# Kernel tuning notes

Measured on AMD Instinct MI355X. Metric: run time of the kernel, lower is better.

## Reference

```python
import jax, jax.numpy as jnp
import numpy as np

NUM_NODES = 10000
IN_DIM = 128
GAT_UNITS = 64
K = 20  # min(20, num_nodes - 1)
NEG_SLOPE = 0.2


def setup_inputs() -> dict:
    key = jax.random.key(0)
    ks = jax.random.split(key, 10)
    s = lambda k, shape, scale: jax.random.normal(k, shape, jnp.float32) * scale
    return {
        "x": s(ks[0], (NUM_NODES, IN_DIM), 1.0),
        "emb": s(ks[1], (NUM_NODES, 16), 1.0),
        "W1": s(ks[2], (IN_DIM, 4, GAT_UNITS), 0.05),
        "a1_src": s(ks[3], (4, GAT_UNITS), 0.05),
        "a1_tgt": s(ks[4], (4, GAT_UNITS), 0.05),
        "b1": jnp.zeros((4 * GAT_UNITS,), jnp.float32),
        "W2": s(ks[5], (4 * GAT_UNITS, 1, GAT_UNITS), 0.05),
        "a2_src": s(ks[6], (1, GAT_UNITS), 0.05),
        "a2_tgt": s(ks[7], (1, GAT_UNITS), 0.05),
        "b2": jnp.zeros((GAT_UNITS,), jnp.float32),
    }


def _build_edges(emb):
    # top-k adjacency from cosine similarity of node embeddings
    norm = emb / jnp.linalg.norm(emb, axis=-1, keepdims=True)
    sim = norm @ norm.T                      # [N, N]
    _, idx = jax.lax.top_k(sim, K)           # [N, K]
    n = emb.shape[0]
    src = jnp.repeat(jnp.arange(n, dtype=jnp.int32), K)
    tgt = idx.reshape(-1).astype(jnp.int32)
    # append self loops (as in the original module)
    loop = jnp.arange(n, dtype=jnp.int32)
    src = jnp.concatenate([src, loop])
    tgt = jnp.concatenate([tgt, loop])
    return src, tgt                          # each [N*(K+1)]


def _gat(x, W, a_src, a_tgt, src, tgt, n):
    # x: [N, F]; W: [F, H, C]; a_*: [H, C]
    h = jnp.einsum("nf,fhc->nhc", x, W)      # [N, H, C]
    e_src = jnp.einsum("nhc,hc->nh", h, a_src)  # [N, H]
    e_tgt = jnp.einsum("nhc,hc->nh", h, a_tgt)  # [N, H]
    logits = jax.nn.leaky_relu(e_src[src] + e_tgt[tgt], NEG_SLOPE)  # [E, H]
    # segment softmax over each source node's neighborhood
    m = jax.ops.segment_max(logits, src, num_segments=n)
    ex = jnp.exp(logits - m[src])
    z = jax.ops.segment_sum(ex, src, num_segments=n)
    alpha = ex / z[src]                      # [E, H]
    msg = alpha[:, :, None] * h[tgt]         # [E, H, C]
    return jax.ops.segment_sum(msg, src, num_segments=n)  # [N, H, C]


def reference(x, emb, W1, a1_src, a1_tgt, b1, W2, a2_src, a2_tgt, b2):
    n = x.shape[0]
    src, tgt = _build_edges(emb)
    # GAT layer 1: 4 heads, concatenated
    h1 = _gat(x, W1, a1_src, a1_tgt, src, tgt, n)        # [N, 4, C]
    h1 = h1.reshape(n, -1) + b1                           # [N, 4C]
    h1 = jax.nn.relu(h1)                                  # (dropout: inference mode)
    # GAT layer 2: 1 head, no concat
    h2 = _gat(h1, W2, a2_src, a2_tgt, src, tgt, n)        # [N, 1, C]
    return h2[:, 0, :] + b2                               # [N, C]
```

## Files before the change

### kernel.cpp

```cpp
#include <hip/hip_runtime.h>
#include <math.h>


#define N_NODES 10000
#define EMB_D   16
#define IN_DIM  128
#define H1      4
#define CDIM    64
#define D1      256
#define K_TOP   20
#define NEIGH   21
#define SROWS   32
#define NTILES  313
#define NTP     320
#define JSPLIT  2
#define HALFT   160
#define CAPM    128
#define GUARD   0.016f

typedef __attribute__((ext_vector_type(8)))  short short8;
typedef __attribute__((ext_vector_type(16))) float f32x16;

__device__ __forceinline__ unsigned monokey(float v) {
  unsigned u = __float_as_uint(v);
  return (u & 0x80000000u) ? ~u : (u | 0x80000000u);
}
__device__ __forceinline__ float invmono(unsigned m) {
  unsigned u = (m & 0x80000000u) ? (m ^ 0x80000000u) : ~m;
  return __uint_as_float(u);
}
__device__ __forceinline__ unsigned short f32_to_bf16(float f) {
  unsigned u = __float_as_uint(f);
  unsigned r = 0x7FFFu + ((u >> 16) & 1u);
  return (unsigned short)((u + r) >> 16);
}

__device__ __forceinline__ float dot16q(float4 qa, float4 qb, float4 qc, float4 qd,
                                        float4 v0, float4 v1, float4 v2, float4 v3) {
  float a = 0.f;
  a = fmaf(qa.x, v0.x, a); a = fmaf(qa.y, v0.y, a);
  a = fmaf(qa.z, v0.z, a); a = fmaf(qa.w, v0.w, a);
  a = fmaf(qb.x, v1.x, a); a = fmaf(qb.y, v1.y, a);
  a = fmaf(qb.z, v1.z, a); a = fmaf(qb.w, v1.w, a);
  a = fmaf(qc.x, v2.x, a); a = fmaf(qc.y, v2.y, a);
  a = fmaf(qc.z, v2.z, a); a = fmaf(qc.w, v2.w, a);
  a = fmaf(qd.x, v3.x, a); a = fmaf(qd.y, v3.y, a);
  a = fmaf(qd.z, v3.z, a); a = fmaf(qd.w, v3.w, a);
  return a;
}

__global__ __launch_bounds__(256) void normalize_kernel(
    const float* __restrict__ emb, float* __restrict__ nrm,
    unsigned short* __restrict__ nrmh) {
  int i = blockIdx.x * 256 + threadIdx.x;
  if (i >= N_NODES) return;
  const float4* p = (const float4*)(emb + (size_t)i * EMB_D);
  float4 v[4];
  float ss = 0.f;
#pragma unroll
  for (int k = 0; k < 4; k++) {
    v[k] = p[k];
    ss = fmaf(v[k].x, v[k].x, ss);
    ss = fmaf(v[k].y, v[k].y, ss);
    ss = fmaf(v[k].z, v[k].z, ss);
    ss = fmaf(v[k].w, v[k].w, ss);
  }
  float nv = sqrtf(ss);
  float4* o = (float4*)(nrm + (size_t)i * EMB_D);
  ushort4* oh = (ushort4*)(nrmh + (size_t)i * EMB_D);
#pragma unroll
  for (int k = 0; k < 4; k++) {
    float4 t;
    t.x = v[k].x / nv; t.y = v[k].y / nv; t.z = v[k].z / nv; t.w = v[k].w / nv;
    o[k] = t;
    ushort4 h;
    h.x = f32_to_bf16(t.x); h.y = f32_to_bf16(t.y);
    h.z = f32_to_bf16(t.z); h.w = f32_to_bf16(t.w);
    oh[k] = h;
  }
}

__global__ __launch_bounds__(512) void sim_topk_part(
    const float* __restrict__ nrm, const unsigned short* __restrict__ nrmh,
    unsigned long long* __restrict__ pkeys) {
  __shared__ unsigned short s_qbf[SROWS * EMB_D];
  __shared__ float s_qf[SROWS * EMB_D];
  __shared__ __align__(16) char s_ovl[SROWS * 256 * 4];
  float (*s_smax)[256] = (float(*)[256])s_ovl;
  unsigned long long (*s_ckey)[CAPM] = (unsigned long long(*)[CAPM])s_ovl;
  __shared__ int s_cid[SROWS][CAPM];
  __shared__ float s_thr[SROWS];
  __shared__ int s_cnt[SROWS];

  int tid = threadIdx.x;
  int w = tid >> 6, lane = tid & 63;
  int lo5 = lane & 31, hi = lane >> 5;
  int row0 = blockIdx.x * SROWS;
  int bh = blockIdx.y;
  int tbase = bh * HALFT;

  if (tid < SROWS * EMB_D) {
    int gi = row0 * EMB_D + tid;
    float v = (gi < N_NODES * EMB_D) ? nrm[gi] : 0.f;
    s_qf[tid] = v;
    s_qbf[tid] = f32_to_bf16(v);
  }
  if (tid < SROWS) s_cnt[tid] = 0;
  __syncthreads();

  short8 afrag = *(const short8*)&s_qbf[lo5 * EMB_D + hi * 8];
  const f32x16 zacc = (f32x16)0.0f;

  float rm[16];
#pragma unroll
  for (int r = 0; r < 16; r++) rm[r] = -INFINITY;

#pragma unroll
  for (int g = 0; g < 5; ++g) {
    int tb = tbase + g * 32 + w * 4;
    int nd[4];
    short8 bf[4];
#pragma unroll
    for (int u = 0; u < 4; u++) {
      nd[u] = (tb + u) * 32 + lo5;
      bf[u] = (short8)(short)0;
      if (nd[u] < N_NODES)
        bf[u] = *(const short8*)&nrmh[(size_t)nd[u] * EMB_D + hi * 8];
    }
#pragma unroll
    for (int u = 0; u < 4; u++) {
      f32x16 acc = __builtin_amdgcn_mfma_f32_32x32x16_bf16(afrag, bf[u], zacc, 0, 0, 0);
      if (nd[u] < N_NODES) {
#pragma unroll
        for (int r = 0; r < 16; r++) rm[r] = fmaxf(rm[r], acc[r]);
      }
    }
  }
#pragma unroll
  for (int r = 0; r < 16; r++) {
    int rl = (r & 3) + 8 * (r >> 2) + 4 * hi;
    s_smax[rl][w * 32 + lo5] = rm[r];
  }
  __syncthreads();

  for (int q = 0; q < 4; q++) {
    int row = w * 4 + q;
    float m01 = fmaxf(s_smax[row][lane], s_smax[row][64 + lane]);
    float m23 = fmaxf(s_smax[row][128 + lane], s_smax[row][192 + lane]);
    unsigned v = monokey(fmaxf(m01, m23));
#pragma unroll
    for (int k = 2; k <= 64; k <<= 1) {
#pragma unroll
      for (int j = k >> 1; j > 0; j >>= 1) {
        unsigned o = __shfl_xor(v, j);
        bool upper = (lane & j) != 0;
        bool ascend = (lane & k) == 0;
        unsigned mx = v > o ? v : o;
        unsigned mn = v > o ? o : v;
        v = (upper == ascend) ? mx : mn;
      }
    }
    unsigned t20 = __shfl(v, 44);
    if (lane == 0)
      s_thr[row] = (row0 + row < N_NODES) ? invmono(t20) - GUARD : INFINITY;
  }
  __syncthreads();

  float thr_r[16];
#pragma unroll
  for (int r = 0; r < 16; r++)
    thr_r[r] = s_thr[(r & 3) + 8 * (r >> 2) + 4 * hi];

#pragma unroll
  for (int g = 0; g < 5; ++g) {
    int tb = tbase + g * 32 + w * 4;
    int nd[4];
    short8 bf[4];
#pragma unroll
    for (int u = 0; u < 4; u++) {
      nd[u] = (tb + u) * 32 + lo5;
      bf[u] = (short8)(short)0;
      if (nd[u] < N_NODES)
        bf[u] = *(const short8*)&nrmh[(size_t)nd[u] * EMB_D + hi * 8];
    }
#pragma unroll
    for (int u = 0; u < 4; u++) {
      f32x16 acc = __builtin_amdgcn_mfma_f32_32x32x16_bf16(afrag, bf[u], zacc, 0, 0, 0);
      if (nd[u] < N_NODES) {
#pragma unroll
        for (int r = 0; r < 16; r++) {
          if (acc[r] >= thr_r[r]) {
            int rl = (r & 3) + 8 * (r >> 2) + 4 * hi;
            int slot = atomicAdd(&s_cnt[rl], 1);
            if (slot < CAPM) s_cid[rl][slot] = nd[u];
          }
        }
      }
    }
  }
  __syncthreads();

  for (int q = 0; q < 4; q++) {
    int row = w * 4 + q;
    if (row0 + row >= N_NODES) continue;
    int M = s_cnt[row];
    if (M > CAPM) continue;
    const float4* qp = (const float4*)&s_qf[row * EMB_D];
    float4 qa = qp[0], qb = qp[1], qc = qp[2], qd = qp[3];
    for (int c = lane; c < M; c += 64) {
      int id = s_cid[row][c];
      const float4* pj = (const float4*)(nrm + (size_t)id * EMB_D);
      float sim = dot16q(qa, qb, qc, qd, pj[0], pj[1], pj[2], pj[3]);
      s_ckey[row][c] = ((unsigned long long)monokey(sim) << 32) |
                       (unsigned long long)(0xFFFFFFFFu - (unsigned)id);
    }
  }
  __syncthreads();

  for (int q = 0; q < 4; q++) {
    int row = w * 4 + q;
    int grow = row0 + row;
    if (grow >= N_NODES) continue;
    unsigned long long* outp = pkeys + ((size_t)grow * JSPLIT + bh) * K_TOP;
    int M = s_cnt[row];
    if (M <= CAPM) {
      for (int c = lane; c < M; c += 64) {
        unsigned long long mykey = s_ckey[row][c];
        int rank = 0;
        for (int i = 0; i < M; i++) rank += (s_ckey[row][i] > mykey) ? 1 : 0;
        if (rank < K_TOP) outp[rank] = mykey;
      }
    } else {
      const float4* qp = (const float4*)&s_qf[row * EMB_D];
      float4 qa = qp[0], qb = qp[1], qc = qp[2], qd = qp[3];
      int j0 = tbase * 32;
      int jend = j0 + HALFT * 32; if (jend > N_NODES) jend = N_NODES;
      unsigned long long prev = ~0ull;
      for (int r = 0; r < K_TOP; r++) {
        unsigned long long best = 0ull;
        for (int j = j0 + lane; j < jend; j += 64) {
          const float4* pj = (const float4*)(nrm + (size_t)j * EMB_D);
          float sim = dot16q(qa, qb, qc, qd, pj[0], pj[1], pj[2], pj[3]);
          unsigned long long key = ((unsigned long long)monokey(sim) << 32) |
                                   (unsigned long long)(0xFFFFFFFFu - (unsigned)j);
          if (key < prev && key > best) best = key;
        }
#pragma unroll
        for (int off = 32; off > 0; off >>= 1) {
          unsigned long long o = __shfl_down(best, off);
          if (o > best) best = o;
        }
        best = __shfl(best, 0);
        prev = best;
        if (lane == 0) outp[r] = best;
      }
    }
  }
}

__global__ __launch_bounds__(256) void topk_merge(
    const unsigned long long* __restrict__ pkeys, int* __restrict__ topk) {
  __shared__ unsigned long long s_k[4][JSPLIT * K_TOP];
  int w = threadIdx.x >> 6, lane = threadIdx.x & 63;
  int row = blockIdx.x * 4 + w;
  const unsigned long long* src = pkeys + (size_t)row * (JSPLIT * K_TOP);
  if (lane < JSPLIT * K_TOP) s_k[w][lane] = src[lane];
  __syncthreads();
  if (lane < JSPLIT * K_TOP) {
    unsigned long long mykey = s_k[w][lane];
    int rank = 0;
    for (int i = 0; i < JSPLIT * K_TOP; i++)
      rank += (s_k[w][i] > mykey) ? 1 : 0;
    if (rank < K_TOP)
      topk[(size_t)row * K_TOP + rank] =
          (int)(0xFFFFFFFFu - (unsigned)(mykey & 0xFFFFFFFFull));
  }
}

__global__ __launch_bounds__(512) void gemm1_kernel(
    const float* __restrict__ A, const float* __restrict__ B,
    const float* __restrict__ a_src, const float* __restrict__ a_tgt,
    float* __restrict__ Cc, float* __restrict__ es, float* __restrict__ et) {
  __shared__ float As[16][IN_DIM];
  int r0 = blockIdx.x * 16;
  int tid = threadIdx.y * 256 + threadIdx.x;
  {
    int rr = tid >> 5;
    int kk = tid & 31;
    ((float4*)&As[rr][0])[kk] = ((const float4*)(A + (size_t)(r0 + rr) * IN_DIM))[kk];
  }
  __syncthreads();
  int col = threadIdx.x;
  int y = threadIdx.y;
  float acc[8] = {0, 0, 0, 0, 0, 0, 0, 0};
#pragma unroll 4
  for (int k = 0; k < IN_DIM; k++) {
    float bv = B[(size_t)k * D1 + col];
#pragma unroll
    for (int r = 0; r < 8; r++) acc[r] = fmaf(As[y * 8 + r][k], bv, acc[r]);
  }
#pragma unroll
  for (int r = 0; r < 8; r++)
    Cc[(size_t)(r0 + y * 8 + r) * D1 + col] = acc[r];
  float as = a_src[col], at = a_tgt[col];
  int h = col >> 6;
#pragma unroll
  for (int r = 0; r < 8; r++) {
    float ps = acc[r] * as, pt = acc[r] * at;
#pragma unroll
    for (int off = 32; off > 0; off >>= 1) {
      ps += __shfl_down(ps, off);
      pt += __shfl_down(pt, off);
    }
    if ((col & 63) == 0) {
      es[(size_t)(r0 + y * 8 + r) * H1 + h] = ps;
      et[(size_t)(r0 + y * 8 + r) * H1 + h] = pt;
    }
  }
}

__global__ __launch_bounds__(256) void gemm2_kernel(
    const float* __restrict__ A, const float* __restrict__ B,
    const float* __restrict__ a_src, const float* __restrict__ a_tgt,
    float* __restrict__ Cc, float* __restrict__ es, float* __restrict__ et) {
  __shared__ float As[16][D1];
  int r0 = blockIdx.x * 16;
  int tid = threadIdx.y * 64 + threadIdx.x;
  for (int e = tid; e < 16 * (D1 / 4); e += 256) {
    int rr = e >> 6;
    int kk = e & 63;
    ((float4*)&As[rr][0])[kk] = ((const float4*)(A + (size_t)(r0 + rr) * D1))[kk];
  }
  __syncthreads();
  int col = threadIdx.x;
  int y = threadIdx.y;
  float acc[4] = {0, 0, 0, 0};
#pragma unroll 4
  for (int k = 0; k < D1; k++) {
    float bv = B[(size_t)k * CDIM + col];
#pragma unroll
    for (int r = 0; r < 4; r++) acc[r] = fmaf(As[y * 4 + r][k], bv, acc[r]);
  }
#pragma unroll
  for (int r = 0; r < 4; r++)
    Cc[(size_t)(r0 + y * 4 + r) * CDIM + col] = acc[r];
  float as = a_src[col], at = a_tgt[col];
#pragma unroll
  for (int r = 0; r < 4; r++) {
    float ps = acc[r] * as, pt = acc[r] * at;
#pragma unroll
    for (int off = 32; off > 0; off >>= 1) {
      ps += __shfl_down(ps, off);
      pt += __shfl_down(pt, off);
    }
    if (col == 0) {
      es[r0 + y * 4 + r] = ps;
      et[r0 + y * 4 + r] = pt;
    }
  }
}

__global__ __launch_bounds__(256) void agg1_kernel(
    const float* __restrict__ h1p, const float* __restrict__ es,
    const float* __restrict__ et, const int* __restrict__ topk,
    const float* __restrict__ b1, float* __restrict__ h1o) {
  int i = blockIdx.x;
  int tid = threadIdx.x;
  __shared__ int nb[NEIGH];
  __shared__ float lg[NEIGH][H1];
  if (tid < K_TOP) nb[tid] = topk[(size_t)i * K_TOP + tid];
  else if (tid == K_TOP) nb[K_TOP] = i;
  __syncthreads();
  if (tid < NEIGH * H1) {
    int e = tid & 3, jj = tid >> 2;
    float L = es[(size_t)i * H1 + e] + et[(size_t)nb[jj] * H1 + e];
    lg[jj][e] = (L > 0.f) ? L : 0.2f * L;
  }
  __syncthreads();
  int h = tid >> 6;
  float m = -INFINITY;
#pragma unroll
  for (int jj = 0; jj < NEIGH; jj++) m = fmaxf(m, lg[jj][h]);
  float z = 0.f, acc = 0.f;
#pragma unroll
  for (int jj = 0; jj < NEIGH; jj++) {
    float w = expf(lg[jj][h] - m);
    z += w;
    acc = fmaf(w, h1p[(size_t)nb[jj] * D1 + tid], acc);
  }
  float o = acc / z + b1[tid];
  h1o[(size_t)i * D1 + tid] = fmaxf(o, 0.f);
}

__global__ __launch_bounds__(256) void agg2_kernel(
    const float* __restrict__ h2p, const float* __restrict__ es,
    const float* __restrict__ et, const int* __restrict__ topk,
    const float* __restrict__ b2, float* __restrict__ out) {
  int tid = threadIdx.x;
  int li = tid >> 6;
  int c = tid & 63;
  int i = blockIdx.x * 4 + li;
  __shared__ int nb[4][NEIGH];
  __shared__ float lg[4][NEIGH];
  if (tid < 4 * NEIGH) {
    int li2 = tid / NEIGH, jj = tid % NEIGH;
    int node = blockIdx.x * 4 + li2;
    nb[li2][jj] = (jj < K_TOP) ? topk[(size_t)node * K_TOP + jj] : node;
  }
  __syncthreads();
  if (tid < 4 * NEIGH) {
    int li2 = tid / NEIGH, jj = tid % NEIGH;
    int node = blockIdx.x * 4 + li2;
    float L = es[node] + et[nb[li2][jj]];
    lg[li2][jj] = (L > 0.f) ? L : 0.2f * L;
  }
  __syncthreads();
  float m = -INFINITY;
#pragma unroll
  for (int jj = 0; jj < NEIGH; jj++) m = fmaxf(m, lg[li][jj]);
  float z = 0.f, acc = 0.f;
#pragma unroll
  for (int jj = 0; jj < NEIGH; jj++) {
    float w = expf(lg[li][jj] - m);
    z += w;
    acc = fmaf(w, h2p[(size_t)nb[li][jj] * CDIM + c], acc);
  }
  out[(size_t)i * CDIM + c] = acc / z + b2[c];
}

extern "C" void kernel_launch(void* const* d_in, const int* in_sizes, int n_in,
                              void* d_out, int out_size, void* d_ws, size_t ws_size,
                              hipStream_t stream) {
  const float* x   = (const float*)d_in[0];
  const float* emb = (const float*)d_in[1];
  const float* W1  = (const float*)d_in[2];
  const float* a1s = (const float*)d_in[3];
  const float* a1t = (const float*)d_in[4];
  const float* b1  = (const float*)d_in[5];
  const float* W2  = (const float*)d_in[6];
  const float* a2s = (const float*)d_in[7];
  const float* a2t = (const float*)d_in[8];
  const float* b2  = (const float*)d_in[9];
  float* out = (float*)d_out;

  size_t off = 0;
  auto alloc = [&](size_t bytes) {
    void* p = (char*)d_ws + off;
    off += (bytes + 255) & ~(size_t)255;
    return p;
  };
  float*          nrm  = (float*)alloc((size_t)N_NODES * EMB_D * sizeof(float));
  unsigned short* nrmh = (unsigned short*)alloc((size_t)N_NODES * EMB_D * sizeof(unsigned short));
  int*   topk = (int*)  alloc((size_t)N_NODES * K_TOP * sizeof(int));
  float* h1p  = (float*)alloc((size_t)N_NODES * D1 * sizeof(float));
  float* e1s  = (float*)alloc((size_t)N_NODES * H1 * sizeof(float));
  float* e1t  = (float*)alloc((size_t)N_NODES * H1 * sizeof(float));
  float* h1   = (float*)alloc((size_t)N_NODES * D1 * sizeof(float));
  float* h2p  = (float*)alloc((size_t)N_NODES * CDIM * sizeof(float));
  float* e2s  = (float*)alloc((size_t)N_NODES * sizeof(float));
  float* e2t  = (float*)alloc((size_t)N_NODES * sizeof(float));
  unsigned long long* pkeys = (unsigned long long*)h1p;
  (void)ws_size; (void)in_sizes; (void)n_in; (void)out_size;

  normalize_kernel<<<(N_NODES + 255) / 256, 256, 0, stream>>>(emb, nrm, nrmh);
  sim_topk_part<<<dim3(NTILES, JSPLIT), 512, 0, stream>>>(nrm, nrmh, pkeys);
  topk_merge<<<N_NODES / 4, 256, 0, stream>>>(pkeys, topk);
  gemm1_kernel<<<N_NODES / 16, dim3(256, 2), 0, stream>>>(x, W1, a1s, a1t, h1p, e1s, e1t);
  agg1_kernel<<<N_NODES, 256, 0, stream>>>(h1p, e1s, e1t, topk, b1, h1);
  gemm2_kernel<<<N_NODES / 16, dim3(64, 4), 0, stream>>>(h1, W2, a2s, a2t, h2p, e2s, e2t);
  agg2_kernel<<<N_NODES / 4, 256, 0, stream>>>(h2p, e2s, e2t, topk, b2, out);
}
```

Baseline: 158.1 us.

## Fuse layer-1 aggregation into layer-2 GEMM and shrink top-k candidate LDS

```diff
diff --git a/kernel.cpp b/kernel.cpp
--- a/kernel.cpp
+++ b/kernel.cpp
@@ -12,10 +12,9 @@
 #define NEIGH   21
 #define SROWS   32
 #define NTILES  313
-#define NTP     320
 #define JSPLIT  2
 #define HALFT   160
-#define CAPM    128
+#define CAPM    96
 #define GUARD   0.016f
 
 typedef __attribute__((ext_vector_type(8)))  short short8;
@@ -85,10 +84,11 @@
     unsigned long long* __restrict__ pkeys) {
   __shared__ unsigned short s_qbf[SROWS * EMB_D];
   __shared__ float s_qf[SROWS * EMB_D];
-  __shared__ __align__(16) char s_ovl[SROWS * 256 * 4];
+  __shared__ __align__(16) char s_ovl[32768];
   float (*s_smax)[256] = (float(*)[256])s_ovl;
   unsigned long long (*s_ckey)[CAPM] = (unsigned long long(*)[CAPM])s_ovl;
-  __shared__ int s_cid[SROWS][CAPM];
+  unsigned short (*s_cid)[CAPM] =
+      (unsigned short(*)[CAPM])(s_ovl + 24576);
   __shared__ float s_thr[SROWS];
   __shared__ int s_cnt[SROWS];
 
@@ -192,7 +192,7 @@
           if (acc[r] >= thr_r[r]) {
             int rl = (r & 3) + 8 * (r >> 2) + 4 * hi;
             int slot = atomicAdd(&s_cnt[rl], 1);
-            if (slot < CAPM) s_cid[rl][slot] = nd[u];
+            if (slot < CAPM) s_cid[rl][slot] = (unsigned short)nd[u];
           }
         }
       }
@@ -293,11 +293,20 @@
   int col = threadIdx.x;
   int y = threadIdx.y;
   float acc[8] = {0, 0, 0, 0, 0, 0, 0, 0};
-#pragma unroll 4
-  for (int k = 0; k < IN_DIM; k++) {
-    float bv = B[(size_t)k * D1 + col];
-#pragma unroll
-    for (int r = 0; r < 8; r++) acc[r] = fmaf(As[y * 8 + r][k], bv, acc[r]);
+  for (int k4 = 0; k4 < IN_DIM / 4; k4++) {
+    float4 a[8];
+#pragma unroll
+    for (int r = 0; r < 8; r++) a[r] = ((const float4*)&As[y * 8 + r][0])[k4];
+    float bv[4];
+#pragma unroll
+    for (int i = 0; i < 4; i++) bv[i] = B[(size_t)(k4 * 4 + i) * D1 + col];
+#pragma unroll
+    for (int r = 0; r < 8; r++) {
+      acc[r] = fmaf(a[r].x, bv[0], acc[r]);
+      acc[r] = fmaf(a[r].y, bv[1], acc[r]);
+      acc[r] = fmaf(a[r].z, bv[2], acc[r]);
+      acc[r] = fmaf(a[r].w, bv[3], acc[r]);
+    }
   }
 #pragma unroll
   for (int r = 0; r < 8; r++)
@@ -319,35 +328,82 @@
   }
 }
 
-__global__ __launch_bounds__(256) void gemm2_kernel(
-    const float* __restrict__ A, const float* __restrict__ B,
+__global__ __launch_bounds__(256) void agg1_gemm2_kernel(
+    const float* __restrict__ h1p, const float* __restrict__ e1s,
+    const float* __restrict__ e1t, const int* __restrict__ topk,
+    const float* __restrict__ b1, const float* __restrict__ B2,
     const float* __restrict__ a_src, const float* __restrict__ a_tgt,
-    float* __restrict__ Cc, float* __restrict__ es, float* __restrict__ et) {
+    float* __restrict__ h2p, float* __restrict__ es, float* __restrict__ et) {
   __shared__ float As[16][D1];
+  __shared__ int nb[16][NEIGH];
+  __shared__ float wv[16][NEIGH][H1];
+  __shared__ float zz[16][H1];
   int r0 = blockIdx.x * 16;
-  int tid = threadIdx.y * 64 + threadIdx.x;
-  for (int e = tid; e < 16 * (D1 / 4); e += 256) {
-    int rr = e >> 6;
-    int kk = e & 63;
-    ((float4*)&As[rr][0])[kk] = ((const float4*)(A + (size_t)(r0 + rr) * D1))[kk];
-  }
-  __syncthreads();
-  int col = threadIdx.x;
-  int y = threadIdx.y;
-  float acc[4] = {0, 0, 0, 0};
-#pragma unroll 4
-  for (int k = 0; k < D1; k++) {
-    float bv = B[(size_t)k * CDIM + col];
-#pragma unroll
-    for (int r = 0; r < 4; r++) acc[r] = fmaf(As[y * 4 + r][k], bv, acc[r]);
+  int tid = threadIdx.x;
+
+  for (int idx = tid; idx < 16 * NEIGH; idx += 256) {
+    int n = idx / NEIGH, jj = idx % NEIGH;
+    nb[n][jj] = (jj < K_TOP) ? topk[(size_t)(r0 + n) * K_TOP + jj] : (r0 + n);
+  }
+  __syncthreads();
+  for (int idx = tid; idx < 16 * NEIGH * H1; idx += 256) {
+    int e = idx & 3, jj = (idx >> 2) % NEIGH, n = idx / (NEIGH * H1);
+    float L = e1s[(size_t)(r0 + n) * H1 + e] + e1t[(size_t)nb[n][jj] * H1 + e];
+    wv[n][jj][e] = (L > 0.f) ? L : 0.2f * L;
+  }
+  __syncthreads();
+  if (tid < 16 * H1) {
+    int n = tid >> 2, h = tid & 3;
+    float m = -INFINITY;
+#pragma unroll
+    for (int jj = 0; jj < NEIGH; jj++) m = fmaxf(m, wv[n][jj][h]);
+    float z = 0.f;
+#pragma unroll
+    for (int jj = 0; jj < NEIGH; jj++) {
+      float wt = expf(wv[n][jj][h] - m);
+      z += wt;
+      wv[n][jj][h] = wt;
+    }
+    zz[n][h] = z;
+  }
+  __syncthreads();
+  {
+    int h = tid >> 6;
+    float bv = b1[tid];
+    for (int n = 0; n < 16; n++) {
+      float acc = 0.f;
+#pragma unroll
+      for (int jj = 0; jj < NEIGH; jj++)
+        acc = fmaf(wv[n][jj][h], h1p[(size_t)nb[n][jj] * D1 + tid], acc);
+      float o = acc / zz[n][h] + bv;
+      As[n][tid] = fmaxf(o, 0.f);
+    }
+  }
+  __syncthreads();
+  int col = tid & 63, y = tid >> 6;
+  float acc4[4] = {0, 0, 0, 0};
+  for (int k4 = 0; k4 < D1 / 4; k4++) {
+    float4 a[4];
+#pragma unroll
+    for (int r = 0; r < 4; r++) a[r] = ((const float4*)&As[y * 4 + r][0])[k4];
+    float bv[4];
+#pragma unroll
+    for (int i = 0; i < 4; i++) bv[i] = B2[(size_t)(k4 * 4 + i) * CDIM + col];
+#pragma unroll
+    for (int r = 0; r < 4; r++) {
+      acc4[r] = fmaf(a[r].x, bv[0], acc4[r]);
+      acc4[r] = fmaf(a[r].y, bv[1], acc4[r]);
+      acc4[r] = fmaf(a[r].z, bv[2], acc4[r]);
+      acc4[r] = fmaf(a[r].w, bv[3], acc4[r]);
+    }
   }
 #pragma unroll
   for (int r = 0; r < 4; r++)
-    Cc[(size_t)(r0 + y * 4 + r) * CDIM + col] = acc[r];
+    h2p[(size_t)(r0 + y * 4 + r) * CDIM + col] = acc4[r];
   float as = a_src[col], at = a_tgt[col];
 #pragma unroll
   for (int r = 0; r < 4; r++) {
-    float ps = acc[r] * as, pt = acc[r] * at;
+    float ps = acc4[r] * as, pt = acc4[r] * at;
 #pragma unroll
     for (int off = 32; off > 0; off >>= 1) {
       ps += __shfl_down(ps, off);
@@ -358,38 +414,6 @@
       et[r0 + y * 4 + r] = pt;
     }
   }
-}
-
-__global__ __launch_bounds__(256) void agg1_kernel(
-    const float* __restrict__ h1p, const float* __restrict__ es,
-    const float* __restrict__ et, const int* __restrict__ topk,
-    const float* __restrict__ b1, float* __restrict__ h1o) {
-  int i = blockIdx.x;
-  int tid = threadIdx.x;
-  __shared__ int nb[NEIGH];
-  __shared__ float lg[NEIGH][H1];
-  if (tid < K_TOP) nb[tid] = topk[(size_t)i * K_TOP + tid];
-  else if (tid == K_TOP) nb[K_TOP] = i;
-  __syncthreads();
-  if (tid < NEIGH * H1) {
-    int e = tid & 3, jj = tid >> 2;
-    float L = es[(size_t)i * H1 + e] + et[(size_t)nb[jj] * H1 + e];
-    lg[jj][e] = (L > 0.f) ? L : 0.2f * L;
-  }
-  __syncthreads();
-  int h = tid >> 6;
-  float m = -INFINITY;
-#pragma unroll
-  for (int jj = 0; jj < NEIGH; jj++) m = fmaxf(m, lg[jj][h]);
-  float z = 0.f, acc = 0.f;
-#pragma unroll
-  for (int jj = 0; jj < NEIGH; jj++) {
-    float w = expf(lg[jj][h] - m);
-    z += w;
-    acc = fmaf(w, h1p[(size_t)nb[jj] * D1 + tid], acc);
-  }
-  float o = acc / z + b1[tid];
-  h1o[(size_t)i * D1 + tid] = fmaxf(o, 0.f);
 }
 
 __global__ __launch_bounds__(256) void agg2_kernel(
@@ -455,7 +479,6 @@
   float* h1p  = (float*)alloc((size_t)N_NODES * D1 * sizeof(float));
   float* e1s  = (float*)alloc((size_t)N_NODES * H1 * sizeof(float));
   float* e1t  = (float*)alloc((size_t)N_NODES * H1 * sizeof(float));
-  float* h1   = (float*)alloc((size_t)N_NODES * D1 * sizeof(float));
   float* h2p  = (float*)alloc((size_t)N_NODES * CDIM * sizeof(float));
   float* e2s  = (float*)alloc((size_t)N_NODES * sizeof(float));
   float* e2t  = (float*)alloc((size_t)N_NODES * sizeof(float));
@@ -466,7 +489,7 @@
   sim_topk_part<<<dim3(NTILES, JSPLIT), 512, 0, stream>>>(nrm, nrmh, pkeys);
   topk_merge<<<N_NODES / 4, 256, 0, stream>>>(pkeys, topk);
   gemm1_kernel<<<N_NODES / 16, dim3(256, 2), 0, stream>>>(x, W1, a1s, a1t, h1p, e1s, e1t);
-  agg1_kernel<<<N_NODES, 256, 0, stream>>>(h1p, e1s, e1t, topk, b1, h1);
-  gemm2_kernel<<<N_NODES / 16, dim3(64, 4), 0, stream>>>(h1, W2, a2s, a2t, h2p, e2s, e2t);
+  agg1_gemm2_kernel<<<N_NODES / 16, 256, 0, stream>>>(h1p, e1s, e1t, topk, b1,
+                                                      W2, a2s, a2t, h2p, e2s, e2t);
   agg2_kernel<<<N_NODES / 4, 256, 0, stream>>>(h2p, e2s, e2t, topk, b2, out);
 }
```

Result: faster. 146.1 us (-7.6%).
